# Kernel optimization log

Measured on AMD Instinct MI355X. Metric: run time of the kernel, lower is better.

Reference implementation:

```python
import jax, jax.numpy as jnp
import numpy as np

B, S, H, NH = 16, 1024, 512, 8
DH = H // NH
EPS = 1e-12
COV_MIN = 1e-24


def _split_heads(x):
    b, s, _ = x.shape
    return x.reshape(b, s, NH, DH).transpose(0, 2, 1, 3)  # [B,NH,S,DH]


def _merge_heads(x):
    b, nh, s, dh = x.shape
    return x.transpose(0, 2, 1, 3).reshape(b, s, nh * dh)


def _layernorm(x, w, b):
    u = jnp.mean(x, -1, keepdims=True)
    s = jnp.mean((x - u) ** 2, -1, keepdims=True)
    return w * ((x - u) / jnp.sqrt(s + EPS)) + b


def _wasserstein(mq, cq, mk, ck):
    # mean part: ||mq_i - mk_j||^2 via matmul expansion
    ret = (-2.0 * jnp.einsum('bhid,bhjd->bhij', mq, mk)
           + jnp.sum(mq ** 2, -1)[..., :, None]
           + jnp.sum(mk ** 2, -1)[..., None, :])
    sq_cq = jnp.sqrt(jnp.clip(cq, COV_MIN))
    sq_ck = jnp.sqrt(jnp.clip(ck, COV_MIN))
    cov_ret = (-2.0 * jnp.einsum('bhid,bhjd->bhij', sq_cq, sq_ck)
               + jnp.sum(cq, -1)[..., :, None]
               + jnp.sum(ck, -1)[..., None, :])
    return ret + cov_ret


def setup_inputs() -> dict:
    key = jax.random.key(0)
    ks = jax.random.split(key, 16)
    d = {
        'x_mean': jax.random.normal(ks[0], (B, S, H), jnp.float32),
        'x_resp_mean': jax.random.normal(ks[1], (B, S, H), jnp.float32),
        'x_cov': jax.random.normal(ks[2], (B, S, H), jnp.float32),
        'x_resp_cov': jax.random.normal(ks[3], (B, S, H), jnp.float32),
    }
    causal = jnp.tril(jnp.ones((S, S), bool))
    d['attn_mask'] = jnp.where(causal, 0.0, -1e4).astype(jnp.float32)[None, None]
    names = ['mq', 'mk', 'mv', 'cq', 'ck', 'cv', 'md', 'cd']
    for i, n in enumerate(names):
        d[n + '_w'] = jax.random.normal(ks[4 + i], (H, H), jnp.float32) * 0.02
        d[n + '_b'] = jnp.zeros((H,), jnp.float32)
    d['ln_w'] = jnp.ones((H,), jnp.float32)
    d['ln_b'] = jnp.zeros((H,), jnp.float32)
    return d


def reference(x_mean, x_resp_mean, x_cov, x_resp_cov, attn_mask,
              mq_w, mq_b, mk_w, mk_b, mv_w, mv_b,
              cq_w, cq_b, ck_w, ck_b, cv_w, cv_b,
              md_w, md_b, cd_w, cd_b, ln_w, ln_b):
    mq = _split_heads(x_mean @ mq_w + mq_b)
    mk = _split_heads(x_mean @ mk_w + mk_b)
    mv = _split_heads(x_resp_mean @ mv_w + mv_b)
    cq = _split_heads(jax.nn.elu(x_cov @ cq_w + cq_b) + 1.0)
    ck = _split_heads(jax.nn.elu(x_cov @ ck_w + ck_b) + 1.0)
    cv = _split_heads(jax.nn.elu(x_resp_cov @ cv_w + cv_b) + 1.0)

    scores = -_wasserstein(mq, cq, mk, ck) / np.sqrt(DH).astype(np.float32)
    scores = scores + attn_mask
    probs = jax.nn.softmax(scores, axis=-1)  # [B,NH,S,S]
    # zero_pad=True: zero out the first query row
    probs = probs.at[:, :, 0, :].set(0.0)

    mean_ctx = _merge_heads(jnp.einsum('bhij,bhjd->bhid', probs, mv))
    cov_ctx = _merge_heads(jnp.einsum('bhij,bhjd->bhid', probs ** 2, cv))

    mean_h = _layernorm(mean_ctx @ md_w + md_b + x_mean, ln_w, ln_b)
    cov_h = _layernorm(cov_ctx @ cd_w + cd_b + x_cov, ln_w, ln_b)
    return mean_h, cov_h, probs
```

## Files before the change

kernel.cpp:

```cpp
#include <hip/hip_runtime.h>
#include <math.h>

#define SLEN 1024
#define NH 8
#define DH 64
#define HDIM 512
#define BATCH 16
#define NROWS (BATCH * SLEN)
#define BHN (BATCH * NH)
#define BHROWS (BHN * SLEN)

typedef short bf16x8 __attribute__((ext_vector_type(8)));
typedef unsigned short u16x8 __attribute__((ext_vector_type(8)));
typedef float f32x4 __attribute__((ext_vector_type(4)));

__device__ __forceinline__ unsigned short f2bf(float f) {
    unsigned u = __float_as_uint(f);
    u += 0x7fffu + ((u >> 16) & 1u);
    return (unsigned short)(u >> 16);
}
__device__ __forceinline__ float bf2f(unsigned short h) {
    return __uint_as_float(((unsigned)h) << 16);
}

__device__ __forceinline__ void gload16(const void *g, void *l) {
    __builtin_amdgcn_global_load_lds(
        (const __attribute__((address_space(1))) unsigned int *)g,
        (__attribute__((address_space(3))) unsigned int *)l,
        16, 0, 0);
}

struct Args {
    const float *xm, *xrm, *xc, *xrc;
    const float *w[8], *bias[8];
    const float *ln_w, *ln_b;
    unsigned short *xbf, *wt;
    float *sums;
    unsigned short *qcat, *kcat, *vcat, *vcat_t, *ctxm, *ctxc;
    float *out_m, *out_c, *probs;
};

__global__ void __launch_bounds__(256) cvt_inputs_k(Args P) {
    const int which = blockIdx.y;
    const float *s = which == 0 ? P.xm : which == 1 ? P.xrm : which == 2 ? P.xc : P.xrc;
    unsigned short *d = P.xbf + (size_t)which * 8388608;
    const long long i = ((long long)blockIdx.x * 256 + threadIdx.x) * 8;
    if (i >= 8388608) return;
    float4 a = *(const float4 *)(s + i);
    float4 b = *(const float4 *)(s + i + 4);
    u16x8 o;
    o[0] = f2bf(a.x); o[1] = f2bf(a.y); o[2] = f2bf(a.z); o[3] = f2bf(a.w);
    o[4] = f2bf(b.x); o[5] = f2bf(b.y); o[6] = f2bf(b.z); o[7] = f2bf(b.w);
    *(u16x8 *)(d + i) = o;
}

__global__ void __launch_bounds__(256) wtrans_k(Args P) {
    const int op = blockIdx.y;
    const float *W = P.w[op];
    unsigned short *WT = P.wt + (size_t)op * 262144;
    const int kt = blockIdx.x >> 3, nt = blockIdx.x & 7;
    __shared__ float Ws[64][65];
    const int t = threadIdx.x;
#pragma unroll
    for (int it = 0; it < 4; ++it) {
        int g = t + 256 * it;
        int k = g >> 4, n4 = (g & 15) * 4;
        float4 v = *(const float4 *)(W + (size_t)(kt * 64 + k) * 512 + nt * 64 + n4);
        Ws[k][n4] = v.x; Ws[k][n4 + 1] = v.y; Ws[k][n4 + 2] = v.z; Ws[k][n4 + 3] = v.w;
    }
    __syncthreads();
#pragma unroll
    for (int it = 0; it < 2; ++it) {
        int g = t + 256 * it;
        int n = g >> 3, kg = (g & 7) * 8;
        u16x8 o;
#pragma unroll
        for (int e = 0; e < 8; ++e) o[e] = f2bf(Ws[kg + e][n]);
        *(u16x8 *)(WT + (size_t)(nt * 64 + n) * 512 + kt * 64 + kg) = o;
    }
}

__global__ void __launch_bounds__(256) mgemm0_k(Args P) {
    const int op = blockIdx.z;
    const int srcidx[6] = {0, 0, 1, 2, 2, 3};
    const unsigned short *Abf = P.xbf + (size_t)srcidx[op] * 8388608;
    const unsigned short *WT = P.wt + (size_t)op * 262144;
    const float *bias = P.bias[op];
    unsigned short *dstb; int doff, act;
    switch (op) {
        case 0: dstb = P.qcat; doff = 0;  act = 0; break;
        case 1: dstb = P.kcat; doff = 0;  act = 0; break;
        case 2: dstb = P.vcat; doff = 0;  act = 0; break;
        case 3: dstb = P.qcat; doff = 64; act = 1; break;
        case 4: dstb = P.kcat; doff = 64; act = 1; break;
        default:dstb = P.vcat; doff = 64; act = 2; break;
    }
    const int lin = blockIdx.y * 4 + blockIdx.x;
    const int xcd = lin & 7, idx = lin >> 3;
    const int m0 = (xcd * 16 + (idx >> 2)) * 128;
    const int n0 = (idx & 3) * 128;

    __shared__ unsigned short As[128][64];
    __shared__ unsigned short Bs[128][64];
    const int t = threadIdx.x;
    const int wid = t >> 6, lane = t & 63;
    const int wm = wid >> 1, wn = wid & 1;
    const int l16 = lane & 15, lq = lane >> 4;
    char *AsB = (char *)&As[0][0];
    char *BsB = (char *)&Bs[0][0];

    f32x4 acc[4][4];
#pragma unroll
    for (int i = 0; i < 4; ++i)
#pragma unroll
        for (int j = 0; j < 4; ++j) acc[i][j] = (f32x4)(0.f);

    for (int k0 = 0; k0 < 512; k0 += 64) {
        __syncthreads();
#pragma unroll
        for (int it = 0; it < 4; ++it) {
            int g = t + 256 * it;
            int r = g >> 3, cg = g & 7;
            int sc = (cg ^ (r & 7)) * 8;
            gload16(Abf + (size_t)(m0 + r) * 512 + k0 + sc, AsB + it * 4096 + wid * 1024);
            gload16(WT + (size_t)(n0 + r) * 512 + k0 + sc, BsB + it * 4096 + wid * 1024);
        }
        __syncthreads();
#pragma unroll
        for (int kk = 0; kk < 2; ++kk) {
            bf16x8 a[4], b[4];
#pragma unroll
            for (int mf = 0; mf < 4; ++mf) {
                int r = wm * 64 + mf * 16 + l16;
                int cg = kk * 4 + lq;
                a[mf] = *(const bf16x8 *)&As[r][(cg ^ (r & 7)) * 8];
            }
#pragma unroll
            for (int nf = 0; nf < 4; ++nf) {
                int r = wn * 64 + nf * 16 + l16;
                int cg = kk * 4 + lq;
                b[nf] = *(const bf16x8 *)&Bs[r][(cg ^ (r & 7)) * 8];
            }
#pragma unroll
            for (int mf = 0; mf < 4; ++mf)
#pragma unroll
                for (int nf = 0; nf < 4; ++nf)
                    acc[mf][nf] = __builtin_amdgcn_mfma_f32_16x16x32_bf16(a[mf], b[nf], acc[mf][nf], 0, 0, 0);
        }
    }

#pragma unroll
    for (int mf = 0; mf < 4; ++mf) {
#pragma unroll
        for (int nf = 0; nf < 4; ++nf) {
#pragma unroll
            for (int r = 0; r < 4; ++r) {
                const int i = m0 + wm * 64 + mf * 16 + lq * 4 + r;
                const int j = n0 + wn * 64 + nf * 16 + l16;
                float v = acc[mf][nf][r] + bias[j];
                if (act == 1) {
                    float e = v > 0.f ? v + 1.f : expf(v);
                    v = sqrtf(fmaxf(e, 1e-24f));
                } else if (act == 2) {
                    v = v > 0.f ? v + 1.f : expf(v);
                }
                const int b_ = i >> 10, s_ = i & (SLEN - 1);
                const int h_ = j >> 6, d_ = j & (DH - 1);
                dstb[((size_t)(b_ * NH + h_) * SLEN + s_) * 128 + doff + d_] = f2bf(v);
            }
        }
    }
}

__global__ void __launch_bounds__(256) vtrans_k(Args P) {
    const int bh = blockIdx.y;
    const int s0 = blockIdx.x * 128;
    __shared__ unsigned short Ts[128][136];
    const unsigned short *src = P.vcat + (size_t)bh * SLEN * 128;
    unsigned short *dst = P.vcat_t + (size_t)bh * 128 * SLEN;
    const int t = threadIdx.x;
#pragma unroll
    for (int it = 0; it < 8; ++it) {
        int g = t + 256 * it;
        int s = g >> 4, dg = g & 15;
        *(u16x8 *)&Ts[s][dg * 8] = *(const u16x8 *)(src + (size_t)(s0 + s) * 128 + dg * 8);
    }
    __syncthreads();
#pragma unroll
    for (int it = 0; it < 8; ++it) {
        int g = t + 256 * it;
        int d = g >> 4, sg = g & 15;
        u16x8 o;
#pragma unroll
        for (int e = 0; e < 8; ++e) o[e] = Ts[sg * 8 + e][d];
        *(u16x8 *)(dst + (size_t)d * SLEN + s0 + sg * 8) = o;
    }
}

__global__ void __launch_bounds__(256) rowsum_k(Args P) {
    const int t = threadIdx.x;
    const int wv = t >> 6, lane = t & 63;
    const long long row = (long long)blockIdx.x * 4 + wv;
    const unsigned short *src = (row < BHROWS) ? P.qcat : P.kcat;
    const long long r = row & (BHROWS - 1);
    const unsigned short *p = src + r * 128;
    float a = bf2f(p[lane]), b = bf2f(p[64 + lane]);
    float v = a * a + b * b;
#pragma unroll
    for (int o = 32; o > 0; o >>= 1) v += __shfl_xor(v, o);
    if (lane == 0) P.sums[row] = v;
}

__global__ void __launch_bounds__(512, 4) flash_k(Args P) {
    const int bh = blockIdx.x;
    const int qt = 31 - (int)blockIdx.y;
    const int q0 = qt * 32;
    __shared__ unsigned short Ep[32][1024];
    __shared__ unsigned short Ks[64][128];
    unsigned short (*Vt)[64] = reinterpret_cast<unsigned short (*)[64]>(&Ks[0][0]);
    float *scr = reinterpret_cast<float *>(&Ks[0][0]);

    const int t = threadIdx.x;
    const int w = t >> 6, lane = t & 63;
    const int l16 = lane & 15, lq = lane >> 4;
    const int mg = w >> 2, q4 = w & 3;

    const unsigned short *qc = P.qcat + (size_t)bh * SLEN * 128;
    const unsigned short *kc = P.kcat + (size_t)bh * SLEN * 128;
    const float *qsum = P.sums + (size_t)bh * SLEN;
    const float *ksum = P.sums + BHROWS + (size_t)bh * SLEN;
    float *pout = P.probs + ((size_t)bh * SLEN + q0) * SLEN;

    const unsigned short *qrow = qc + (size_t)(q0 + mg * 16 + l16) * 128;
    bf16x8 qfr[4];
#pragma unroll
    for (int kk = 0; kk < 4; ++kk) qfr[kk] = *(const bf16x8 *)(qrow + (kk * 4 + lq) * 8);
    float qs[4];
#pragma unroll
    for (int r = 0; r < 4; ++r) qs[r] = qsum[q0 + mg * 16 + lq * 4 + r];

    const int nkt = (q0 >> 6) + 1;
    const int rK = q4 * 16 + l16;
    float tpart[4] = {0.f, 0.f, 0.f, 0.f};
    const float C = 0.18033688f;

    const int sr0 = t >> 4, sg = t & 15;
    const int sr1 = sr0 + 32;
    bf16x8 kreg0 = *(const bf16x8 *)(kc + (size_t)sr0 * 128 + sg * 8);
    bf16x8 kreg1 = *(const bf16x8 *)(kc + (size_t)sr1 * 128 + sg * 8);
    float ksreg = ksum[rK];

    for (int kt = 0; kt < nkt; ++kt) {
        __syncthreads();
        *(bf16x8 *)&Ks[sr0][(sg ^ (sr0 & 7)) * 8] = kreg0;
        *(bf16x8 *)&Ks[sr1][(sg ^ (sr1 & 7)) * 8] = kreg1;
        if (kt + 1 < nkt) {
            kreg0 = *(const bf16x8 *)(kc + (size_t)((kt + 1) * 64 + sr0) * 128 + sg * 8);
            kreg1 = *(const bf16x8 *)(kc + (size_t)((kt + 1) * 64 + sr1) * 128 + sg * 8);
        }
        __syncthreads();

        const float ksv = ksreg;
        if (kt + 1 < nkt) ksreg = ksum[(kt + 1) * 64 + rK];

        __builtin_amdgcn_s_setprio(1);
        f32x4 acc = (f32x4)(0.f);
#pragma unroll
        for (int kk = 0; kk < 4; ++kk) {
            bf16x8 b = *(const bf16x8 *)&Ks[rK][((kk * 4 + lq) ^ (rK & 7)) * 8];
            acc = __builtin_amdgcn_mfma_f32_16x16x32_bf16(qfr[kk], b, acc, 0, 0, 0);
        }
        __builtin_amdgcn_s_setprio(0);
        const int j = kt * 64 + rK;
#pragma unroll
        for (int r = 0; r < 4; ++r) {
            const int row = mg * 16 + lq * 4 + r;
            const int i = q0 + row;
            float sv = (2.f * acc[r] - qs[r] - ksv) * C;
            float e = (j <= i) ? exp2f(sv) : 0.f;
            tpart[r] += e;
            Ep[row][(((j >> 3) ^ (row & 7)) << 3) | (j & 7)] = f2bf(e);
        }
    }

    {
        const int zrow = t >> 4;
        f32x4 z = (f32x4)(0.f);
        for (int c4 = nkt * 16 + (t & 15); c4 < 256; c4 += 16)
            *(f32x4 *)(pout + (size_t)zrow * SLEN + c4 * 4) = z;
    }

#pragma unroll
    for (int o = 1; o < 16; o <<= 1)
#pragma unroll
        for (int r = 0; r < 4; ++r) tpart[r] += __shfl_xor(tpart[r], o);
    __syncthreads();
    if (l16 == 0) {
#pragma unroll
        for (int r = 0; r < 4; ++r) scr[q4 * 32 + mg * 16 + lq * 4 + r] = tpart[r];
    }
    __syncthreads();
    float invP;
    {
        const int row = t >> 4;
        const float T = scr[row] + scr[32 + row] + scr[64 + row] + scr[96 + row];
        invP = (q0 + row == 0) ? 0.f : (1.f / T);
    }
    float invC[4];
#pragma unroll
    for (int r = 0; r < 4; ++r) {
        const int row = mg * 16 + lq * 4 + r;
        const float T = scr[row] + scr[32 + row] + scr[64 + row] + scr[96 + row];
        invC[r] = (q0 + row == 0) ? 0.f : (1.f / T);
    }
    __syncthreads();

    const int cov = q4 >> 1;
    f32x4 pacc[2];
    pacc[0] = (f32x4)(0.f); pacc[1] = (f32x4)(0.f);
    const unsigned short *vtg = P.vcat_t + (size_t)bh * 128 * SLEN;
    const int vr0 = t >> 3, vg = t & 7;
    const int vr1 = vr0 + 64;
    bf16x8 vreg0 = *(const bf16x8 *)(vtg + (size_t)vr0 * SLEN + vg * 8);
    bf16x8 vreg1 = *(const bf16x8 *)(vtg + (size_t)vr1 * SLEN + vg * 8);

    for (int kt = 0; kt < nkt; ++kt) {
        __syncthreads();
        *(bf16x8 *)&Vt[vr0][(vg ^ (vr0 & 7)) * 8] = vreg0;
        *(bf16x8 *)&Vt[vr1][(vg ^ (vr1 & 7)) * 8] = vreg1;
        if (kt + 1 < nkt) {
            vreg0 = *(const bf16x8 *)(vtg + (size_t)vr0 * SLEN + (kt + 1) * 64 + vg * 8);
            vreg1 = *(const bf16x8 *)(vtg + (size_t)vr1 * SLEN + (kt + 1) * 64 + vg * 8);
        }
        __syncthreads();

        __builtin_amdgcn_s_setprio(1);
#pragma unroll
        for (int kk = 0; kk < 2; ++kk) {
            const int row = mg * 16 + l16;
            const int gg = (kt * 8) + kk * 4 + lq;
            bf16x8 af = *(const bf16x8 *)&Ep[row][((gg ^ (row & 7)) << 3)];
            if (cov) {
                u16x8 u = (u16x8)af, sq;
#pragma unroll
                for (int e = 0; e < 8; ++e) {
                    float f = bf2f(u[e]);
                    sq[e] = f2bf(f * f);
                }
                af = (bf16x8)sq;
            }
#pragma unroll
            for (int nf = 0; nf < 2; ++nf) {
                const int d = q4 * 32 + nf * 16 + l16;
                bf16x8 bf = *(const bf16x8 *)&Vt[d][((kk * 4 + lq) ^ (d & 7)) * 8];
                pacc[nf] = __builtin_amdgcn_mfma_f32_16x16x32_bf16(af, bf, pacc[nf], 0, 0, 0);
            }
        }
        __builtin_amdgcn_s_setprio(0);

        {
            const int prow = t >> 4, slot = t & 15;
            const int col = kt * 64 + slot * 4;
            const int g = col >> 3, o4 = (slot & 1) * 4;
            u16x8 v = *(const u16x8 *)&Ep[prow][((g ^ (prow & 7)) << 3)];
            f32x4 ov;
            if (kt == nkt - 1) {
                const int i = q0 + prow;
#pragma unroll
                for (int e = 0; e < 4; ++e)
                    ov[e] = (col + e <= i) ? bf2f(v[o4 + e]) * invP : 0.f;
            } else {
#pragma unroll
                for (int e = 0; e < 4; ++e)
                    ov[e] = bf2f(v[o4 + e]) * invP;
            }
            *(f32x4 *)(pout + (size_t)prow * SLEN + col) = ov;
        }
    }

    unsigned short *dst = cov ? P.ctxc : P.ctxm;
    const int b_ = bh >> 3, h_ = bh & 7;
#pragma unroll
    for (int nf = 0; nf < 2; ++nf) {
#pragma unroll
        for (int r = 0; r < 4; ++r) {
            const int row = mg * 16 + lq * 4 + r;
            const int s_ = q0 + row;
            const float scale = cov ? invC[r] * invC[r] : invC[r];
            dst[((size_t)b_ * SLEN + s_) * HDIM + h_ * 64 + (q4 & 1) * 32 + nf * 16 + l16] =
                f2bf(pacc[nf][r] * scale);
        }
    }
}

__global__ void __launch_bounds__(512, 4) mgemm_ln_k(Args P) {
    const int op = blockIdx.y;
    const unsigned short *Abf = op ? P.ctxc : P.ctxm;
    const unsigned short *WT = P.wt + (size_t)(6 + op) * 262144;
    const float *bias = P.bias[6 + op];
    const float *resid = op ? P.xc : P.xm;
    float *out = op ? P.out_c : P.out_m;
    const int m0 = blockIdx.x * 64;

    __shared__ unsigned short As[64][64];
    __shared__ unsigned short Bs[512][64];
    __shared__ float Red[64][4][2];

    const int t = threadIdx.x;
    const int w = t >> 6, lane = t & 63;
    const int wm = w >> 2, wn = w & 3;
    const int l16 = lane & 15, lq = lane >> 4;
    char *AsB = (char *)&As[0][0];
    char *BsB = (char *)&Bs[0][0];

    f32x4 acc[2][8];
#pragma unroll
    for (int mf = 0; mf < 2; ++mf)
#pragma unroll
        for (int nf = 0; nf < 8; ++nf) acc[mf][nf] = (f32x4)(0.f);

    for (int k0 = 0; k0 < 512; k0 += 64) {
        __syncthreads();
        {
            int r = t >> 3, cg = t & 7;
            int sc = (cg ^ (r & 7)) * 8;
            gload16(Abf + (size_t)(m0 + r) * 512 + k0 + sc, AsB + w * 1024);
        }
#pragma unroll
        for (int it = 0; it < 8; ++it) {
            int g = t + 512 * it;
            int r = g >> 3, cg = g & 7;
            int sc = (cg ^ (r & 7)) * 8;
            gload16(WT + (size_t)r * 512 + k0 + sc, BsB + it * 8192 + w * 1024);
        }
        __syncthreads();
#pragma unroll
        for (int kk = 0; kk < 2; ++kk) {
            bf16x8 a[2];
#pragma unroll
            for (int mf = 0; mf < 2; ++mf) {
                int r = wm * 32 + mf * 16 + l16;
                a[mf] = *(const bf16x8 *)&As[r][((kk * 4 + lq) ^ (r & 7)) * 8];
            }
#pragma unroll
            for (int nf = 0; nf < 8; ++nf) {
                int rn = wn * 128 + nf * 16 + l16;
                bf16x8 b = *(const bf16x8 *)&Bs[rn][((kk * 4 + lq) ^ (rn & 7)) * 8];
#pragma unroll
                for (int mf = 0; mf < 2; ++mf)
                    acc[mf][nf] = __builtin_amdgcn_mfma_f32_16x16x32_bf16(a[mf], b, acc[mf][nf], 0, 0, 0);
            }
        }
    }

    float bv[8];
#pragma unroll
    for (int nf = 0; nf < 8; ++nf) bv[nf] = bias[wn * 128 + nf * 16 + l16];

    float s0[2][4], s1[2][4];
#pragma unroll
    for (int mf = 0; mf < 2; ++mf)
#pragma unroll
        for (int r = 0; r < 4; ++r) { s0[mf][r] = 0.f; s1[mf][r] = 0.f; }

#pragma unroll
    for (int mf = 0; mf < 2; ++mf) {
#pragma unroll
        for (int r = 0; r < 4; ++r) {
            const int i = m0 + wm * 32 + mf * 16 + lq * 4 + r;
            const float *rrow = resid + (size_t)i * HDIM + wn * 128 + l16;
#pragma unroll
            for (int nf = 0; nf < 8; ++nf) {
                float x = acc[mf][nf][r] + bv[nf] + rrow[nf * 16];
                acc[mf][nf][r] = x;
                s0[mf][r] += x;
                s1[mf][r] += x * x;
            }
        }
    }
#pragma unroll
    for (int o = 1; o < 16; o <<= 1)
#pragma unroll
        for (int mf = 0; mf < 2; ++mf)
#pragma unroll
            for (int r = 0; r < 4; ++r) {
                s0[mf][r] += __shfl_xor(s0[mf][r], o);
                s1[mf][r] += __shfl_xor(s1[mf][r], o);
            }
    if (l16 == 0) {
#pragma unroll
        for (int mf = 0; mf < 2; ++mf)
#pragma unroll
            for (int r = 0; r < 4; ++r) {
                const int row = wm * 32 + mf * 16 + lq * 4 + r;
                Red[row][wn][0] = s0[mf][r];
                Red[row][wn][1] = s1[mf][r];
            }
    }
    __syncthreads();

    float lnw[8], lnb[8];
#pragma unroll
    for (int nf = 0; nf < 8; ++nf) {
        const int j = wn * 128 + nf * 16 + l16;
        lnw[nf] = P.ln_w[j]; lnb[nf] = P.ln_b[j];
    }
#pragma unroll
    for (int mf = 0; mf < 2; ++mf) {
#pragma unroll
        for (int r = 0; r < 4; ++r) {
            const int row = wm * 32 + mf * 16 + lq * 4 + r;
            const int i = m0 + row;
            const float S  = Red[row][0][0] + Red[row][1][0] + Red[row][2][0] + Red[row][3][0];
            const float SS = Red[row][0][1] + Red[row][1][1] + Red[row][2][1] + Red[row][3][1];
            const float mean = S * (1.f / 512.f);
            const float var = SS * (1.f / 512.f) - mean * mean;
            const float inv = 1.f / sqrtf(var + 1e-12f);
            float *orow = out + (size_t)i * HDIM + wn * 128 + l16;
#pragma unroll
            for (int nf = 0; nf < 8; ++nf)
                orow[nf * 16] = lnw[nf] * ((acc[mf][nf][r] - mean) * inv) + lnb[nf];
        }
    }
}

extern "C" void kernel_launch(void *const *d_in, const int *in_sizes, int n_in,
                              void *d_out, int out_size, void *d_ws, size_t ws_size,
                              hipStream_t stream) {
    (void)in_sizes; (void)n_in; (void)out_size; (void)ws_size;
    Args P;
    P.xm  = (const float *)d_in[0];
    P.xrm = (const float *)d_in[1];
    P.xc  = (const float *)d_in[2];
    P.xrc = (const float *)d_in[3];
    for (int i = 0; i < 8; ++i) {
        P.w[i]    = (const float *)d_in[5 + 2 * i];
        P.bias[i] = (const float *)d_in[6 + 2 * i];
    }
    P.ln_w = (const float *)d_in[21];
    P.ln_b = (const float *)d_in[22];

    char *ws = (char *)d_ws;
    P.xbf    = (unsigned short *)(ws);
    P.vcat_t = (unsigned short *)(ws);
    P.ctxm   = (unsigned short *)(ws + 33554432);
    P.ctxc   = (unsigned short *)(ws + 50331648);
    P.wt     = (unsigned short *)(ws + 67108864);
    P.sums   = (float *)(ws + 71303168);
    P.qcat   = (unsigned short *)(ws + 72351744);
    P.kcat   = (unsigned short *)(ws + 105906176);
    P.vcat   = (unsigned short *)(ws + 139460608);

    P.out_m = (float *)d_out;
    P.out_c = (float *)d_out + 8388608;
    P.probs = (float *)d_out + 16777216;

    cvt_inputs_k<<<dim3(4096, 4), dim3(256), 0, stream>>>(P);
    wtrans_k<<<dim3(64, 8), dim3(256), 0, stream>>>(P);
    mgemm0_k<<<dim3(4, 128, 6), dim3(256), 0, stream>>>(P);
    vtrans_k<<<dim3(8, 128), dim3(256), 0, stream>>>(P);
    rowsum_k<<<dim3(65536), dim3(256), 0, stream>>>(P);
    flash_k<<<dim3(128, 32), dim3(512), 0, stream>>>(P);
    mgemm_ln_k<<<dim3(256, 2), dim3(512), 0, stream>>>(P);
}
```

Before: 466.5 us.

## Fuse V transpose and row-sum computation into projection GEMM epilogue

The projection GEMM epilogue now writes V directly in transposed layout and computes per-row squared sums for Q/K halves via lane shuffles, removing the separate vtrans and rowsum kernels. Sums are stored as four partial arrays (mean/cov for q and k) and added in the attention kernel. This saves two kernel launches and the extra global round trips over qcat/kcat/vcat, at the cost of scattered 8-byte transposed stores and extra epilogue work.

```diff
diff --git a/kernel.cpp b/kernel.cpp
--- a/kernel.cpp
+++ b/kernel.cpp
@@ -12,6 +12,7 @@
 
 typedef short bf16x8 __attribute__((ext_vector_type(8)));
 typedef unsigned short u16x8 __attribute__((ext_vector_type(8)));
+typedef unsigned short u16x4 __attribute__((ext_vector_type(4)));
 typedef float f32x4 __attribute__((ext_vector_type(4)));
 
 __device__ __forceinline__ unsigned short f2bf(float f) {
@@ -36,7 +37,7 @@
     const float *ln_w, *ln_b;
     unsigned short *xbf, *wt;
     float *sums;
-    unsigned short *qcat, *kcat, *vcat, *vcat_t, *ctxm, *ctxc;
+    unsigned short *qcat, *kcat, *vcat_t, *ctxm, *ctxc;
     float *out_m, *out_c, *probs;
 };
 
@@ -90,10 +91,10 @@
     switch (op) {
         case 0: dstb = P.qcat; doff = 0;  act = 0; break;
         case 1: dstb = P.kcat; doff = 0;  act = 0; break;
-        case 2: dstb = P.vcat; doff = 0;  act = 0; break;
+        case 2: dstb = nullptr; doff = 0;  act = 0; break;
         case 3: dstb = P.qcat; doff = 64; act = 1; break;
         case 4: dstb = P.kcat; doff = 64; act = 1; break;
-        default:dstb = P.vcat; doff = 64; act = 2; break;
+        default:dstb = nullptr; doff = 64; act = 2; break;
     }
     const int lin = blockIdx.y * 4 + blockIdx.x;
     const int xcd = lin & 7, idx = lin >> 3;
@@ -149,66 +150,76 @@
         }
     }
 
-#pragma unroll
-    for (int mf = 0; mf < 4; ++mf) {
-#pragma unroll
-        for (int nf = 0; nf < 4; ++nf) {
+    const int b_ = m0 >> 10;
+    const int srow0 = m0 & 1023;
+    const bool isV = (op == 2 || op == 5);
+
+    if (isV) {
+        unsigned short *vt = P.vcat_t;
+#pragma unroll
+        for (int mf = 0; mf < 4; ++mf) {
+#pragma unroll
+            for (int nf = 0; nf < 4; ++nf) {
+                const int j = n0 + wn * 64 + nf * 16 + l16;
+                const int h_ = j >> 6, dd = doff + (j & 63);
+                u16x4 pk;
+#pragma unroll
+                for (int r = 0; r < 4; ++r) {
+                    float v = acc[mf][nf][r] + bias[j];
+                    if (act == 2) v = v > 0.f ? v + 1.f : expf(v);
+                    pk[r] = f2bf(v);
+                }
+                const int s_ = srow0 + wm * 64 + mf * 16 + lq * 4;
+                *(u16x4 *)(vt + ((size_t)(b_ * NH + h_) * 128 + dd) * SLEN + s_) = pk;
+            }
+        }
+    } else {
+        float rs[4][4];
+#pragma unroll
+        for (int mf = 0; mf < 4; ++mf)
+#pragma unroll
+            for (int r = 0; r < 4; ++r) rs[mf][r] = 0.f;
+
+#pragma unroll
+        for (int mf = 0; mf < 4; ++mf) {
+#pragma unroll
+            for (int nf = 0; nf < 4; ++nf) {
+                const int j = n0 + wn * 64 + nf * 16 + l16;
+                const int h_ = j >> 6, d_ = j & 63;
+#pragma unroll
+                for (int r = 0; r < 4; ++r) {
+                    float v = acc[mf][nf][r] + bias[j];
+                    if (act == 1) {
+                        float e = v > 0.f ? v + 1.f : expf(v);
+                        v = sqrtf(fmaxf(e, 1e-24f));
+                    }
+                    unsigned short hb = f2bf(v);
+                    const int s_ = srow0 + wm * 64 + mf * 16 + lq * 4 + r;
+                    dstb[((size_t)(b_ * NH + h_) * SLEN + s_) * 128 + doff + d_] = hb;
+                    const float vb = bf2f(hb);
+                    rs[mf][r] += vb * vb;
+                }
+            }
+        }
+        float *sdst = P.sums +
+            (size_t)((op == 0) ? 0 : (op == 3) ? 1 : (op == 1) ? 2 : 3) * BHROWS;
+        const int h_ = (n0 >> 6) + wn;
+#pragma unroll
+        for (int mf = 0; mf < 4; ++mf) {
 #pragma unroll
             for (int r = 0; r < 4; ++r) {
-                const int i = m0 + wm * 64 + mf * 16 + lq * 4 + r;
-                const int j = n0 + wn * 64 + nf * 16 + l16;
-                float v = acc[mf][nf][r] + bias[j];
-                if (act == 1) {
-                    float e = v > 0.f ? v + 1.f : expf(v);
-                    v = sqrtf(fmaxf(e, 1e-24f));
-                } else if (act == 2) {
-                    v = v > 0.f ? v + 1.f : expf(v);
+                float x = rs[mf][r];
+                x += __shfl_xor(x, 1);
+                x += __shfl_xor(x, 2);
+                x += __shfl_xor(x, 4);
+                x += __shfl_xor(x, 8);
+                if (l16 == 0) {
+                    const int s_ = srow0 + wm * 64 + mf * 16 + lq * 4 + r;
+                    sdst[(size_t)(b_ * NH + h_) * SLEN + s_] = x;
                 }
-                const int b_ = i >> 10, s_ = i & (SLEN - 1);
-                const int h_ = j >> 6, d_ = j & (DH - 1);
-                dstb[((size_t)(b_ * NH + h_) * SLEN + s_) * 128 + doff + d_] = f2bf(v);
-            }
-        }
-    }
-}
-
-__global__ void __launch_bounds__(256) vtrans_k(Args P) {
-    const int bh = blockIdx.y;
-    const int s0 = blockIdx.x * 128;
-    __shared__ unsigned short Ts[128][136];
-    const unsigned short *src = P.vcat + (size_t)bh * SLEN * 128;
-    unsigned short *dst = P.vcat_t + (size_t)bh * 128 * SLEN;
-    const int t = threadIdx.x;
-#pragma unroll
-    for (int it = 0; it < 8; ++it) {
-        int g = t + 256 * it;
-        int s = g >> 4, dg = g & 15;
-        *(u16x8 *)&Ts[s][dg * 8] = *(const u16x8 *)(src + (size_t)(s0 + s) * 128 + dg * 8);
-    }
-    __syncthreads();
-#pragma unroll
-    for (int it = 0; it < 8; ++it) {
-        int g = t + 256 * it;
-        int d = g >> 4, sg = g & 15;
-        u16x8 o;
-#pragma unroll
-        for (int e = 0; e < 8; ++e) o[e] = Ts[sg * 8 + e][d];
-        *(u16x8 *)(dst + (size_t)d * SLEN + s0 + sg * 8) = o;
-    }
-}
-
-__global__ void __launch_bounds__(256) rowsum_k(Args P) {
-    const int t = threadIdx.x;
-    const int wv = t >> 6, lane = t & 63;
-    const long long row = (long long)blockIdx.x * 4 + wv;
-    const unsigned short *src = (row < BHROWS) ? P.qcat : P.kcat;
-    const long long r = row & (BHROWS - 1);
-    const unsigned short *p = src + r * 128;
-    float a = bf2f(p[lane]), b = bf2f(p[64 + lane]);
-    float v = a * a + b * b;
-#pragma unroll
-    for (int o = 32; o > 0; o >>= 1) v += __shfl_xor(v, o);
-    if (lane == 0) P.sums[row] = v;
+            }
+        }
+    }
 }
 
 __global__ void __launch_bounds__(512, 4) flash_k(Args P) {
@@ -227,8 +238,10 @@
 
     const unsigned short *qc = P.qcat + (size_t)bh * SLEN * 128;
     const unsigned short *kc = P.kcat + (size_t)bh * SLEN * 128;
-    const float *qsum = P.sums + (size_t)bh * SLEN;
-    const float *ksum = P.sums + BHROWS + (size_t)bh * SLEN;
+    const float *qm_p = P.sums + (size_t)bh * SLEN;
+    const float *qc_p = qm_p + BHROWS;
+    const float *km_p = P.sums + 2 * (size_t)BHROWS + (size_t)bh * SLEN;
+    const float *kc_p = km_p + BHROWS;
     float *pout = P.probs + ((size_t)bh * SLEN + q0) * SLEN;
 
     const unsigned short *qrow = qc + (size_t)(q0 + mg * 16 + l16) * 128;
@@ -237,7 +250,10 @@
     for (int kk = 0; kk < 4; ++kk) qfr[kk] = *(const bf16x8 *)(qrow + (kk * 4 + lq) * 8);
     float qs[4];
 #pragma unroll
-    for (int r = 0; r < 4; ++r) qs[r] = qsum[q0 + mg * 16 + lq * 4 + r];
+    for (int r = 0; r < 4; ++r) {
+        const int i = q0 + mg * 16 + lq * 4 + r;
+        qs[r] = qm_p[i] + qc_p[i];
+    }
 
     const int nkt = (q0 >> 6) + 1;
     const int rK = q4 * 16 + l16;
@@ -248,7 +264,7 @@
     const int sr1 = sr0 + 32;
     bf16x8 kreg0 = *(const bf16x8 *)(kc + (size_t)sr0 * 128 + sg * 8);
     bf16x8 kreg1 = *(const bf16x8 *)(kc + (size_t)sr1 * 128 + sg * 8);
-    float ksreg = ksum[rK];
+    float ksreg = km_p[rK] + kc_p[rK];
 
     for (int kt = 0; kt < nkt; ++kt) {
         __syncthreads();
@@ -261,7 +277,10 @@
         __syncthreads();
 
         const float ksv = ksreg;
-        if (kt + 1 < nkt) ksreg = ksum[(kt + 1) * 64 + rK];
+        if (kt + 1 < nkt) {
+            const int jn = (kt + 1) * 64 + rK;
+            ksreg = km_p[jn] + kc_p[jn];
+        }
 
         __builtin_amdgcn_s_setprio(1);
         f32x4 acc = (f32x4)(0.f);
@@ -542,14 +561,13 @@
 
     char *ws = (char *)d_ws;
     P.xbf    = (unsigned short *)(ws);
-    P.vcat_t = (unsigned short *)(ws);
     P.ctxm   = (unsigned short *)(ws + 33554432);
     P.ctxc   = (unsigned short *)(ws + 50331648);
     P.wt     = (unsigned short *)(ws + 67108864);
     P.sums   = (float *)(ws + 71303168);
-    P.qcat   = (unsigned short *)(ws + 72351744);
-    P.kcat   = (unsigned short *)(ws + 105906176);
-    P.vcat   = (unsigned short *)(ws + 139460608);
+    P.qcat   = (unsigned short *)(ws + 73400320);
+    P.kcat   = (unsigned short *)(ws + 106954752);
+    P.vcat_t = (unsigned short *)(ws + 140509184);
 
     P.out_m = (float *)d_out;
     P.out_c = (float *)d_out + 8388608;
@@ -558,8 +576,6 @@
     cvt_inputs_k<<<dim3(4096, 4), dim3(256), 0, stream>>>(P);
     wtrans_k<<<dim3(64, 8), dim3(256), 0, stream>>>(P);
     mgemm0_k<<<dim3(4, 128, 6), dim3(256), 0, stream>>>(P);
-    vtrans_k<<<dim3(8, 128), dim3(256), 0, stream>>>(P);
-    rowsum_k<<<dim3(65536), dim3(256), 0, stream>>>(P);
     flash_k<<<dim3(128, 32), dim3(512), 0, stream>>>(P);
     mgemm_ln_k<<<dim3(256, 2), dim3(512), 0, stream>>>(P);
 }
```

Result: faster. 448.7 us (-3.8%).
